# Kernel tuning notes

Hardware: AMD Instinct MI355X
Metric: run time of the kernel (lower is better)

Reference implementation:

```python
import jax, jax.numpy as jnp
import numpy as np

COST_CLASS = 1.0
COST_BBOX = 1.0
COST_GIOU = 1.0
COST_MASK_CE = 1.0
COST_MASK_DICE = 1.0
ALPHA = 0.25   # hardcoded in forward (focal alpha)
GAMMA = 2.0


def box_cxcywh_to_xyxy(b):
    cx, cy, w, h = jnp.split(b, 4, axis=-1)
    return jnp.concatenate([cx - 0.5 * w, cy - 0.5 * h, cx + 0.5 * w, cy + 0.5 * h], axis=-1)


def generalized_box_iou(b1, b2):
    # b1 [N,4], b2 [M,4] in xyxy -> [N,M]
    a1 = (b1[:, 2] - b1[:, 0]) * (b1[:, 3] - b1[:, 1])
    a2 = (b2[:, 2] - b2[:, 0]) * (b2[:, 3] - b2[:, 1])
    lt = jnp.maximum(b1[:, None, :2], b2[None, :, :2])
    rb = jnp.minimum(b1[:, None, 2:], b2[None, :, 2:])
    wh = jnp.clip(rb - lt, 0.0)
    inter = wh[..., 0] * wh[..., 1]
    union = a1[:, None] + a2[None, :] - inter
    iou = inter / union
    ltc = jnp.minimum(b1[:, None, :2], b2[None, :, :2])
    rbc = jnp.maximum(b1[:, None, 2:], b2[None, :, 2:])
    whc = jnp.clip(rbc - ltc, 0.0)
    area = whc[..., 0] * whc[..., 1]
    return iou - (area - union) / area


def point_sample_bilinear(masks, coords):
    # masks [N,H,W], coords [P,2] in [0,1] (x,y); grid_sample align_corners=False,
    # zero padding: pixel = coord*size - 0.5. Fully batched over N and P.
    H, W = masks.shape[-2:]
    x = coords[:, 0] * W - 0.5
    y = coords[:, 1] * H - 0.5
    x0 = jnp.floor(x); y0 = jnp.floor(y)
    wx = x - x0; wy = y - y0
    x0i = x0.astype(jnp.int32); y0i = y0.astype(jnp.int32)
    def g(yi, xi):
        valid = ((xi >= 0) & (xi < W) & (yi >= 0) & (yi < H)).astype(masks.dtype)
        v = masks[:, jnp.clip(yi, 0, H - 1), jnp.clip(xi, 0, W - 1)]  # [N,P]
        return v * valid
    return (g(y0i, x0i) * (1 - wy) * (1 - wx) + g(y0i, x0i + 1) * (1 - wy) * wx
            + g(y0i + 1, x0i) * wy * (1 - wx) + g(y0i + 1, x0i + 1) * wy * wx)


def point_sample_nearest(masks, coords):
    H, W = masks.shape[-2:]
    xi = jnp.round(coords[:, 0] * W - 0.5).astype(jnp.int32)
    yi = jnp.round(coords[:, 1] * H - 0.5).astype(jnp.int32)
    valid = ((xi >= 0) & (xi < W) & (yi >= 0) & (yi < H)).astype(masks.dtype)
    return masks[:, jnp.clip(yi, 0, H - 1), jnp.clip(xi, 0, W - 1)] * valid


def _cost_single(logits, boxes, labels, tboxes, pmasks, tmasks, pts):
    # logits [Q,C], boxes [Q,4], labels [T], tboxes [T,4],
    # pmasks [Q,H,W], tmasks [T,H,W] (0/1 int), pts [P,2]
    prob = jax.nn.sigmoid(logits)
    neg_cost = (1 - ALPHA) * prob ** GAMMA * (-jax.nn.log_sigmoid(-logits))
    pos_cost = ALPHA * (1 - prob) ** GAMMA * (-jax.nn.log_sigmoid(logits))
    cost_class = jnp.take(pos_cost, labels, axis=1) - jnp.take(neg_cost, labels, axis=1)  # [Q,T]
    giou = generalized_box_iou(box_cxcywh_to_xyxy(boxes), box_cxcywh_to_xyxy(tboxes))
    cost_bbox = jnp.abs(boxes[:, None, :] - tboxes[None, :, :]).sum(-1)  # L1 cdist
    C = COST_BBOX * cost_bbox + COST_CLASS * cost_class - COST_GIOU * giou
    # batched point sampling (replaces per-query / per-target python loops)
    pm = point_sample_bilinear(pmasks, pts)                    # [Q,P]
    tm = point_sample_nearest(tmasks.astype(pmasks.dtype), pts)  # [T,P]
    P = pm.shape[-1]
    # batch_sigmoid_ce_loss: pairwise BCE-with-logits, mean over points
    pos_ce = jax.nn.softplus(-pm)  # loss if target==1
    neg_ce = jax.nn.softplus(pm)   # loss if target==0
    ce = (pos_ce @ tm.T + neg_ce @ (1.0 - tm).T) / P
    # batch_dice_loss
    sm = jax.nn.sigmoid(pm)
    num = 2.0 * (sm @ tm.T)
    den = sm.sum(-1)[:, None] + tm.sum(-1)[None, :]
    dice = 1.0 - (num + 1.0) / (den + 1.0)
    C = C + COST_MASK_CE * ce + COST_MASK_DICE * dice
    # replicate C[C.isinf()|C.isnan()] = 2*max
    finite = jnp.isfinite(C)
    mx = jnp.max(jnp.where(finite, C, -jnp.inf))
    return jnp.where(finite, C, 2.0 * mx)


def setup_inputs() -> dict:
    key = jax.random.key(0)
    ks = jax.random.split(key, 7)
    bs, Q, C, T, H, W = 2, 900, 91, 100, 128, 128
    P = H * W // 16  # mask_point_sample_ratio = 16
    return {
        "pred_logits": jax.random.normal(ks[0], (bs, Q, C), jnp.float32),
        "pred_boxes": jax.random.uniform(ks[1], (bs, Q, 4), jnp.float32),
        "tgt_labels": jax.random.randint(ks[2], (bs, T), 0, C, jnp.int32),
        "tgt_boxes": jax.random.uniform(ks[3], (bs, T, 4), jnp.float32),
        "pred_masks": jax.random.normal(ks[4], (bs, Q, H, W), jnp.float32),
        "tgt_masks": jax.random.randint(ks[5], (bs, T, H, W), 0, 2, jnp.int32),
        "point_coords": jax.random.uniform(ks[6], (bs, P, 2), jnp.float32),
    }


def reference(pred_logits, pred_boxes, tgt_labels, tgt_boxes, pred_masks, tgt_masks, point_coords):
    # Returns the per-image matching cost matrices [bs, Q, T]; the CPU-side
    # Hungarian solve (scipy linear_sum_assignment) consumes these.
    return jax.vmap(_cost_single)(pred_logits, pred_boxes, tgt_labels, tgt_boxes,
                                  pred_masks, tgt_masks, point_coords)
```

## Files before the change

kernel.cpp:

```cpp
#include <hip/hip_runtime.h>
#include <math.h>

#define QN 900
#define TN 100
#define CN 91
#define PN 1024
#define HWD 128
#define BS 2

typedef float f32x2 __attribute__((ext_vector_type(2)));

__device__ __forceinline__ float sigmoidf_(float x) {
    return 1.0f / (1.0f + __expf(-x));
}
__device__ __forceinline__ float softplusf_(float x) {
    return fmaxf(x, 0.0f) + __logf(1.0f + __expf(-fabsf(x)));
}
__device__ __forceinline__ unsigned bfhi(float f) {
    unsigned u = __float_as_uint(f);
    return (u + 0x7FFFu + ((u >> 16) & 1u)) & 0xFFFF0000u;
}

__global__ __launch_bounds__(256) void prep_kernel(
    const float2* __restrict__ coords, const int* __restrict__ tmasks,
    unsigned* __restrict__ tmw, float* __restrict__ tmsum)
{
    __shared__ int cnt[4];
    const int bx = blockIdx.x;
    const int tid = threadIdx.x;
    const int wv = tid >> 6, lane = tid & 63;
    const int b = bx / TN, t = bx % TN;
    const int* m = tmasks + (size_t)(b * TN + t) * (HWD * HWD);
    int addr[4]; unsigned vld[4];
#pragma unroll
    for (int c = 0; c < 4; ++c) {
        float2 cd = coords[b * PN + c * 256 + tid];
        int xi = (int)rintf(cd.x * (float)HWD - 0.5f);
        int yi = (int)rintf(cd.y * (float)HWD - 0.5f);
        vld[c] = (xi >= 0) & (xi < HWD) & (yi >= 0) & (yi < HWD);
        addr[c] = min(max(yi, 0), HWD - 1) * HWD + min(max(xi, 0), HWD - 1);
    }
    int rv[4];
#pragma unroll
    for (int c = 0; c < 4; ++c) rv[c] = m[addr[c]];
    int mycnt = 0;
#pragma unroll
    for (int c = 0; c < 4; ++c) {
        unsigned long long bal = __ballot(vld[c] && (rv[c] != 0));
        if (lane == 0) {
            tmw[(size_t)(b * TN + t) * 32 + c * 8 + wv * 2 + 0] = (unsigned)(bal & 0xFFFFFFFFull);
            tmw[(size_t)(b * TN + t) * 32 + c * 8 + wv * 2 + 1] = (unsigned)(bal >> 32);
            mycnt += __popcll(bal);
        }
    }
    if (lane == 0) cnt[wv] = mycnt;
    __syncthreads();
    if (tid == 0)
        tmsum[b * TN + t] = (float)((cnt[0] + cnt[1]) + (cnt[2] + cnt[3]));
}

__global__ __launch_bounds__(256, 4) void main_kernel(
    const float* __restrict__ logits, const float4* __restrict__ pboxes,
    const int* __restrict__ labels, const float4* __restrict__ tboxes,
    const float* __restrict__ pmasks, const float2* __restrict__ coords,
    const unsigned* __restrict__ tmw, const float* __restrict__ tmsum_,
    float* __restrict__ out, float* __restrict__ blockmax,
    int* __restrict__ badflag)
{
    __shared__ unsigned pl[PN];
    __shared__ float part[8][32][9];
    __shared__ float sred[8];
    __shared__ float mred[256];
    __shared__ int sbad;

    const int bq = blockIdx.x;
    const int b = bq / QN, q = bq - b * QN;
    const int tid = threadIdx.x;
    const int wv = tid >> 6, lane = tid & 63;
    const int pc = tid >> 5, ts = tid & 31;
    const float* mask = pmasks + (size_t)bq * (HWD * HWD);

    if (tid == 0) sbad = 0;

    int ar0[4], ar1[4];
    int x0a[4];
    float wxa[4], wya[4];
    unsigned fl[4];
#pragma unroll
    for (int c = 0; c < 4; ++c) {
        float2 cd = coords[b * PN + c * 256 + tid];
        float x = cd.x * (float)HWD - 0.5f;
        float y = cd.y * (float)HWD - 0.5f;
        float fx = floorf(x), fy = floorf(y);
        int x0 = (int)fx, y0 = (int)fy;
        int x1 = x0 + 1, y1 = y0 + 1;
        wxa[c] = x - fx; wya[c] = y - fy;
        x0a[c] = x0;
        int xl = min(max(x0, 0), HWD - 2);
        int yc0 = min(max(y0, 0), HWD - 1), yc1 = min(max(y1, 0), HWD - 1);
        ar0[c] = yc0 * HWD + xl;
        ar1[c] = yc1 * HWD + xl;
        fl[c] = (unsigned)((x0 >= 0) & (x0 < HWD))
              | ((unsigned)((x1 >= 0) & (x1 < HWD)) << 1)
              | ((unsigned)((y0 >= 0) & (y0 < HWD)) << 2)
              | ((unsigned)((y1 >= 0) & (y1 < HWD)) << 3);
    }

    f32x2 p0[4], p1[4];
#pragma unroll
    for (int c = 0; c < 4; ++c) {
        p0[c] = *(const f32x2*)(mask + ar0[c]);
        p1[c] = *(const f32x2*)(mask + ar1[c]);
    }

    const unsigned* rowb = tmw + (size_t)b * TN * 32;
    unsigned w0[4], w1[4], w2[4], w3[4];
#pragma unroll
    for (int g = 0; g < 4; ++g) {
        w0[g] = rowb[(ts +  0) * 32 + pc * 4 + g];
        w1[g] = rowb[(ts + 32) * 32 + pc * 4 + g];
        w2[g] = rowb[(ts + 64) * 32 + pc * 4 + g];
        w3[g] = (ts + 96 < TN) ? rowb[(ts + 96) * 32 + pc * 4 + g] : 0u;
    }
    float lg = 0.f, tsum = 0.f;
    float4 tb = make_float4(0, 0, 0, 0), pb = make_float4(0, 0, 0, 0);
    if (tid < TN) {
        int lab = labels[b * TN + tid];
        lg = logits[(size_t)(b * QN + q) * CN + lab];
        tsum = tmsum_[b * TN + tid];
        tb = tboxes[b * TN + tid];
        pb = pboxes[b * QN + q];
    }

    float lsp = 0.f, lsm = 0.f;
#pragma unroll
    for (int c = 0; c < 4; ++c) {
        const bool x0hi = (x0a[c] >= HWD - 1);
        const bool x1lo = (x0a[c] < 0);
        float v00 = x0hi ? p0[c].y : p0[c].x;
        float v01 = x1lo ? p0[c].x : p0[c].y;
        float v10 = x0hi ? p1[c].y : p1[c].x;
        float v11 = x1lo ? p1[c].x : p1[c].y;
        const bool bx0 = fl[c] & 1u, bx1 = fl[c] & 2u, by0 = fl[c] & 4u, by1 = fl[c] & 8u;
        v00 = (by0 && bx0) ? v00 : 0.f;
        v01 = (by0 && bx1) ? v01 : 0.f;
        v10 = (by1 && bx0) ? v10 : 0.f;
        v11 = (by1 && bx1) ? v11 : 0.f;
        float wx = wxa[c], wy = wya[c];
        float pm = (v00 * (1.f - wx) + v01 * wx) * (1.f - wy) +
                   (v10 * (1.f - wx) + v11 * wx) * wy;
        float sg = sigmoidf_(pm);
        lsp += softplusf_(pm);
        lsm += sg;
        pl[c * 256 + tid] = bfhi(pm) | (bfhi(sg) >> 16);
    }
    for (int off = 32; off > 0; off >>= 1) {
        lsp += __shfl_down(lsp, off);
        lsm += __shfl_down(lsm, off);
    }
    if (lane == 0) { sred[wv * 2 + 0] = lsp; sred[wv * 2 + 1] = lsm; }
    __syncthreads();
    float s_sp = (sred[0] + sred[2]) + (sred[4] + sred[6]);
    float s_sm = (sred[1] + sred[3]) + (sred[5] + sred[7]);

    float a0 = 0, a1 = 0, a2 = 0, a3 = 0, a4 = 0, a5 = 0, a6 = 0, a7 = 0;
#pragma unroll
    for (int g = 0; g < 4; ++g) {
        unsigned u0 = w0[g], u1 = w1[g], u2 = w2[g], u3 = w3[g];
        int p0i = pc * 128 + g * 32;
#pragma unroll
        for (int jj = 0; jj < 8; ++jj) {
            uint4 u = *(const uint4*)&pl[p0i + jj * 4];
#pragma unroll
            for (int k = 0; k < 4; ++k) {
                unsigned uv = (k == 0) ? u.x : (k == 1) ? u.y : (k == 2) ? u.z : u.w;
                float pmv = __uint_as_float(uv & 0xFFFF0000u);
                float sgv = __uint_as_float(uv << 16);
                float f0 = (float)((u0 >> k) & 1u);
                float f1 = (float)((u1 >> k) & 1u);
                float f2 = (float)((u2 >> k) & 1u);
                float f3 = (float)((u3 >> k) & 1u);
                a0 = fmaf(pmv, f0, a0); a1 = fmaf(sgv, f0, a1);
                a2 = fmaf(pmv, f1, a2); a3 = fmaf(sgv, f1, a3);
                a4 = fmaf(pmv, f2, a4); a5 = fmaf(sgv, f2, a5);
                a6 = fmaf(pmv, f3, a6); a7 = fmaf(sgv, f3, a7);
            }
            u0 >>= 4; u1 >>= 4; u2 >>= 4; u3 >>= 4;
        }
    }
    part[pc][ts][0] = a0; part[pc][ts][1] = a1;
    part[pc][ts][2] = a2; part[pc][ts][3] = a3;
    part[pc][ts][4] = a4; part[pc][ts][5] = a5;
    part[pc][ts][6] = a6; part[pc][ts][7] = a7;
    __syncthreads();

    float val = -INFINITY;
    if (tid < TN) {
        int t = tid, tss = t & 31, kk = t >> 5;
        float apm = 0.f, asg = 0.f;
#pragma unroll
        for (int pp = 0; pp < 8; ++pp) {
            apm += part[pp][tss][kk * 2 + 0];
            asg += part[pp][tss][kk * 2 + 1];
        }
        float ce = (s_sp - apm) * (1.0f / (float)PN);
        float dice = 1.0f - (2.0f * asg + 1.0f) / (s_sm + tsum + 1.0f);

        float pr = sigmoidf_(lg);
        float cls = 0.25f * (1.f - pr) * (1.f - pr) * softplusf_(-lg)
                  - 0.75f * pr * pr * softplusf_(lg);

        float l1 = fabsf(pb.x - tb.x) + fabsf(pb.y - tb.y) +
                   fabsf(pb.z - tb.z) + fabsf(pb.w - tb.w);

        float px1 = pb.x - 0.5f * pb.z, py1 = pb.y - 0.5f * pb.w;
        float px2 = pb.x + 0.5f * pb.z, py2 = pb.y + 0.5f * pb.w;
        float tx1 = tb.x - 0.5f * tb.z, ty1 = tb.y - 0.5f * tb.w;
        float tx2 = tb.x + 0.5f * tb.z, ty2 = tb.y + 0.5f * tb.w;
        float A1 = (px2 - px1) * (py2 - py1);
        float A2 = (tx2 - tx1) * (ty2 - ty1);
        float iw = fmaxf(fminf(px2, tx2) - fmaxf(px1, tx1), 0.f);
        float ih = fmaxf(fminf(py2, ty2) - fmaxf(py1, ty1), 0.f);
        float inter = iw * ih;
        float uni = A1 + A2 - inter;
        float iou = inter / uni;
        float cw = fmaxf(fmaxf(px2, tx2) - fminf(px1, tx1), 0.f);
        float chh = fmaxf(fmaxf(py2, ty2) - fminf(py1, ty1), 0.f);
        float area = cw * chh;
        float giou = iou - (area - uni) / area;

        float Cv = l1 + cls - giou + ce + dice;
        out[(size_t)(b * QN + q) * TN + t] = Cv;
        if (isfinite(Cv)) val = Cv;
        else sbad = 1;
    }
    mred[tid] = val;
    __syncthreads();
    if (tid < 64) {
        float m = fmaxf(fmaxf(mred[tid], mred[tid + 64]),
                        fmaxf(mred[tid + 128], mred[tid + 192]));
        for (int off = 32; off > 0; off >>= 1)
            m = fmaxf(m, __shfl_down(m, off));
        if (tid == 0) { blockmax[bq] = m; badflag[bq] = sbad; }
    }
}

__global__ __launch_bounds__(128) void fix_kernel(float* __restrict__ out,
                                                  const float* __restrict__ blockmax,
                                                  const int* __restrict__ badflag)
{
    const int bq = blockIdx.x;
    if (badflag[bq] == 0) return;
    const int tid = threadIdx.x;
    if (tid >= TN) return;
    const int b = bq / QN;
    float v = out[(size_t)bq * TN + tid];
    if (!isfinite(v)) {
        float m = -INFINITY;
        for (int k = 0; k < QN; ++k) m = fmaxf(m, blockmax[b * QN + k]);
        out[(size_t)bq * TN + tid] = 2.0f * m;
    }
}

extern "C" void kernel_launch(void* const* d_in, const int* in_sizes, int n_in,
                              void* d_out, int out_size, void* d_ws, size_t ws_size,
                              hipStream_t stream) {
    const float* logits  = (const float*)d_in[0];
    const float4* pboxes = (const float4*)d_in[1];
    const int* labels    = (const int*)d_in[2];
    const float4* tboxes = (const float4*)d_in[3];
    const float* pmasks  = (const float*)d_in[4];
    const int* tmasks    = (const int*)d_in[5];
    const float* coords  = (const float*)d_in[6];
    float* out = (float*)d_out;

    char* ws = (char*)d_ws;
    unsigned* tmw   = (unsigned*)(ws);
    float* tmsum    = (float*)(ws + 25600);
    float* blockmax = (float*)(ws + 26400);
    int* badflag    = (int*)(ws + 33600);

    hipLaunchKernelGGL(prep_kernel, dim3(BS * TN), dim3(256), 0, stream,
                       (const float2*)coords, tmasks, tmw, tmsum);
    hipLaunchKernelGGL(main_kernel, dim3(BS * QN), dim3(256), 0, stream,
                       logits, pboxes, labels, tboxes, pmasks, (const float2*)coords,
                       tmw, tmsum, out, blockmax, badflag);
    hipLaunchKernelGGL(fix_kernel, dim3(BS * QN), dim3(128), 0, stream,
                       out, blockmax, badflag);
}
```

Baseline: 53.24 us.

## Sort sample points by mask address and precompute a packed sampling table

Adds a bitonic-sort kernel that orders the sample points of each image by their bilinear gather address. It writes a packed per-point table holding both row addresses, validity flags, the weights and the nearest-neighbour address. The main and prep kernels read this table instead of recomputing coordinates, so the per-block mask gathers touch memory in address order with better cache-line locality. The cost is one extra kernel launch with a serial sort, and the point order is permuted, which the point-sum reductions must tolerate.

```diff
diff --git a/kernel.cpp b/kernel.cpp
--- a/kernel.cpp
+++ b/kernel.cpp
@@ -21,8 +21,72 @@
     return (u + 0x7FFFu + ((u >> 16) & 1u)) & 0xFFFF0000u;
 }
 
+__global__ __launch_bounds__(1024) void sort_kernel(
+    const float2* __restrict__ coords, uint4* __restrict__ table)
+{
+    __shared__ unsigned key[PN];
+    const int b = blockIdx.x;
+    const int tid = threadIdx.x;
+
+    {
+        float2 cd = coords[b * PN + tid];
+        float x = cd.x * (float)HWD - 0.5f;
+        float y = cd.y * (float)HWD - 0.5f;
+        int x0 = (int)floorf(x);
+        int y0 = (int)floorf(y);
+        int xl = min(max(x0, 0), HWD - 2);
+        int yc0 = min(max(y0, 0), HWD - 1);
+        unsigned ar0 = (unsigned)(yc0 * HWD + xl);
+        key[tid] = (ar0 << 10) | (unsigned)tid;
+    }
+    for (int k = 2; k <= PN; k <<= 1) {
+        for (int j = k >> 1; j > 0; j >>= 1) {
+            __syncthreads();
+            int ixj = tid ^ j;
+            if (ixj > tid) {
+                unsigned a = key[tid], c = key[ixj];
+                bool up = ((tid & k) == 0);
+                if ((a > c) == up) { key[tid] = c; key[ixj] = a; }
+            }
+        }
+    }
+    __syncthreads();
+
+    const int idx = (int)(key[tid] & 1023u);
+    float2 cd = coords[b * PN + idx];
+    float x = cd.x * (float)HWD - 0.5f;
+    float y = cd.y * (float)HWD - 0.5f;
+    float fx = floorf(x), fy = floorf(y);
+    int x0 = (int)fx, y0 = (int)fy;
+    int y1 = y0 + 1;
+    float wx = x - fx, wy = y - fy;
+    bool bx0, bx1;
+    int xl;
+    if (x0 < 0)            { xl = 0;       bx0 = true;  bx1 = false; wx = 1.f - wx; }
+    else if (x0 >= HWD-1)  { xl = HWD - 2; bx0 = false; bx1 = true;  wx = 1.f - wx; }
+    else                   { xl = x0;      bx0 = true;  bx1 = true; }
+    bool by0 = (y0 >= 0) & (y0 < HWD);
+    bool by1 = (y1 >= 0) & (y1 < HWD);
+    int yc0 = min(max(y0, 0), HWD - 1), yc1 = min(max(y1, 0), HWD - 1);
+    unsigned ar0 = (unsigned)(yc0 * HWD + xl);
+    unsigned ar1 = (unsigned)(yc1 * HWD + xl);
+    unsigned fl = (unsigned)bx0 | ((unsigned)bx1 << 1) |
+                  ((unsigned)by0 << 2) | ((unsigned)by1 << 3);
+    int xi = (int)rintf(cd.x * (float)HWD - 0.5f);
+    int yi = (int)rintf(cd.y * (float)HWD - 0.5f);
+    unsigned nvalid = (xi >= 0) & (xi < HWD) & (yi >= 0) & (yi < HWD);
+    unsigned naddr = (unsigned)(min(max(yi, 0), HWD - 1) * HWD + min(max(xi, 0), HWD - 1));
+
+    uint4 te;
+    te.x = ar0 | (ar1 << 14) | (fl << 28);
+    te.y = __float_as_uint(wx);
+    te.z = __float_as_uint(wy);
+    te.w = naddr | (nvalid << 14);
+    table[b * PN + tid] = te;
+}
+
 __global__ __launch_bounds__(256) void prep_kernel(
-    const float2* __restrict__ coords, const int* __restrict__ tmasks,
+    const uint4* __restrict__ table, const int* __restrict__ tmasks,
     unsigned* __restrict__ tmw, float* __restrict__ tmsum)
 {
     __shared__ int cnt[4];
@@ -34,11 +98,9 @@
     int addr[4]; unsigned vld[4];
 #pragma unroll
     for (int c = 0; c < 4; ++c) {
-        float2 cd = coords[b * PN + c * 256 + tid];
-        int xi = (int)rintf(cd.x * (float)HWD - 0.5f);
-        int yi = (int)rintf(cd.y * (float)HWD - 0.5f);
-        vld[c] = (xi >= 0) & (xi < HWD) & (yi >= 0) & (yi < HWD);
-        addr[c] = min(max(yi, 0), HWD - 1) * HWD + min(max(xi, 0), HWD - 1);
+        unsigned w = table[b * PN + c * 256 + tid].w;
+        addr[c] = (int)(w & 16383u);
+        vld[c] = w >> 14;
     }
     int rv[4];
 #pragma unroll
@@ -62,7 +124,7 @@
 __global__ __launch_bounds__(256, 4) void main_kernel(
     const float* __restrict__ logits, const float4* __restrict__ pboxes,
     const int* __restrict__ labels, const float4* __restrict__ tboxes,
-    const float* __restrict__ pmasks, const float2* __restrict__ coords,
+    const float* __restrict__ pmasks, const uint4* __restrict__ table,
     const unsigned* __restrict__ tmw, const float* __restrict__ tmsum_,
     float* __restrict__ out, float* __restrict__ blockmax,
     int* __restrict__ badflag)
@@ -82,28 +144,17 @@
 
     if (tid == 0) sbad = 0;
 
+    unsigned fl[4];
+    float wxa[4], wya[4];
     int ar0[4], ar1[4];
-    int x0a[4];
-    float wxa[4], wya[4];
-    unsigned fl[4];
-#pragma unroll
-    for (int c = 0; c < 4; ++c) {
-        float2 cd = coords[b * PN + c * 256 + tid];
-        float x = cd.x * (float)HWD - 0.5f;
-        float y = cd.y * (float)HWD - 0.5f;
-        float fx = floorf(x), fy = floorf(y);
-        int x0 = (int)fx, y0 = (int)fy;
-        int x1 = x0 + 1, y1 = y0 + 1;
-        wxa[c] = x - fx; wya[c] = y - fy;
-        x0a[c] = x0;
-        int xl = min(max(x0, 0), HWD - 2);
-        int yc0 = min(max(y0, 0), HWD - 1), yc1 = min(max(y1, 0), HWD - 1);
-        ar0[c] = yc0 * HWD + xl;
-        ar1[c] = yc1 * HWD + xl;
-        fl[c] = (unsigned)((x0 >= 0) & (x0 < HWD))
-              | ((unsigned)((x1 >= 0) & (x1 < HWD)) << 1)
-              | ((unsigned)((y0 >= 0) & (y0 < HWD)) << 2)
-              | ((unsigned)((y1 >= 0) & (y1 < HWD)) << 3);
+#pragma unroll
+    for (int c = 0; c < 4; ++c) {
+        uint4 te = table[b * PN + c * 256 + tid];
+        ar0[c] = (int)(te.x & 16383u);
+        ar1[c] = (int)((te.x >> 14) & 16383u);
+        fl[c] = te.x >> 28;
+        wxa[c] = __uint_as_float(te.y);
+        wya[c] = __uint_as_float(te.z);
     }
 
     f32x2 p0[4], p1[4];
@@ -135,17 +186,11 @@
     float lsp = 0.f, lsm = 0.f;
 #pragma unroll
     for (int c = 0; c < 4; ++c) {
-        const bool x0hi = (x0a[c] >= HWD - 1);
-        const bool x1lo = (x0a[c] < 0);
-        float v00 = x0hi ? p0[c].y : p0[c].x;
-        float v01 = x1lo ? p0[c].x : p0[c].y;
-        float v10 = x0hi ? p1[c].y : p1[c].x;
-        float v11 = x1lo ? p1[c].x : p1[c].y;
         const bool bx0 = fl[c] & 1u, bx1 = fl[c] & 2u, by0 = fl[c] & 4u, by1 = fl[c] & 8u;
-        v00 = (by0 && bx0) ? v00 : 0.f;
-        v01 = (by0 && bx1) ? v01 : 0.f;
-        v10 = (by1 && bx0) ? v10 : 0.f;
-        v11 = (by1 && bx1) ? v11 : 0.f;
+        float v00 = (by0 && bx0) ? p0[c].x : 0.f;
+        float v01 = (by0 && bx1) ? p0[c].y : 0.f;
+        float v10 = (by1 && bx0) ? p1[c].x : 0.f;
+        float v11 = (by1 && bx1) ? p1[c].y : 0.f;
         float wx = wxa[c], wy = wya[c];
         float pm = (v00 * (1.f - wx) + v01 * wx) * (1.f - wy) +
                    (v10 * (1.f - wx) + v11 * wx) * wy;
@@ -279,11 +324,14 @@
     float* tmsum    = (float*)(ws + 25600);
     float* blockmax = (float*)(ws + 26400);
     int* badflag    = (int*)(ws + 33600);
-
+    uint4* table    = (uint4*)(ws + 40960);
+
+    hipLaunchKernelGGL(sort_kernel, dim3(BS), dim3(1024), 0, stream,
+                       (const float2*)coords, table);
     hipLaunchKernelGGL(prep_kernel, dim3(BS * TN), dim3(256), 0, stream,
-                       (const float2*)coords, tmasks, tmw, tmsum);
+                       table, tmasks, tmw, tmsum);
     hipLaunchKernelGGL(main_kernel, dim3(BS * QN), dim3(256), 0, stream,
-                       logits, pboxes, labels, tboxes, pmasks, (const float2*)coords,
+                       logits, pboxes, labels, tboxes, pmasks, table,
                        tmw, tmsum, out, blockmax, badflag);
     hipLaunchKernelGGL(fix_kernel, dim3(BS * QN), dim3(128), 0, stream,
                        out, blockmax, badflag);
```

New measurement: 55.90 us. 1.05x slower.
